# Kernel optimization log

Hardware: AMD Instinct MI355X
Metric: run time of the kernel (lower is better)

## Reference

```python
import jax, jax.numpy as jnp
import numpy as np

KH, KW = 5, 5  # filter_size
PAD_H, PAD_W = KH // 2, KW // 2


def setup_inputs() -> dict:
    key = jax.random.key(0)
    k1, k2 = jax.random.split(key)
    n, c, h, w = 4, 3, 180, 320
    filter_prod = KH * KW          # 25
    upsampling_square = 16
    x = jax.random.normal(k1, (n, c, h, w), dtype=jnp.float32)
    filters = jax.random.uniform(k2, (n, filter_prod, upsampling_square, h, w), dtype=jnp.float32)
    return {"x": x, "filters": filters}


def _unfold(x):
    # Equivalent of conv2d with a grouped identity (eye) expansion filter:
    # extracts kh*kw patches per channel in row-major (i, j) kernel order.
    n, c, h, w = x.shape
    xp = jnp.pad(x, ((0, 0), (0, 0), (PAD_H, PAD_H), (PAD_W, PAD_W)))
    # (n, c, kh*kw, h, w); fixed 25-iteration loop over kernel taps.
    patches = jnp.stack(
        [xp[:, :, i:i + h, j:j + w] for i in range(KH) for j in range(KW)],
        axis=2,
    )
    return patches


def reference(x, filters):
    n, filter_prod, upsampling_square, h, w = filters.shape
    patches = _unfold(x)  # (n, 3, filter_prod, h, w)
    out = jnp.einsum('ncphw,npuhw->ncuhw', patches, filters)
    return out.reshape(n, 3 * upsampling_square, h, w)
```

## Files before the change

kernel.cpp:

```cpp
#include <hip/hip_runtime.h>


#define HH 180
#define WW 320
#define CC 3
#define UU 16
#define NN 4

__global__ __launch_bounds__(256) void duf_kernel(
    const float* __restrict__ x,
    const float* __restrict__ filters,
    float* __restrict__ out)
{
    const int HW = HH * WW;
    int idx = blockIdx.x * 256 + threadIdx.x;
    const int total = NN * UU * HW;
    if (idx >= total) return;

    int w = idx % WW;
    int t = idx / WW;
    int h = t % HH;
    t /= HH;
    int u = t % UU;
    int n = t / UU;

    const float* fptr = filters + ((size_t)((n * 25) * UU + u) * HH + h) * WW + w;
    const float* xbase = x + (size_t)(n * CC) * HW;

    float acc0 = 0.f, acc1 = 0.f, acc2 = 0.f;

    #pragma unroll
    for (int i = 0; i < 5; ++i) {
        int hi = h + i - 2;
        bool rowv = (hi >= 0) & (hi < HH);
        int hic = min(max(hi, 0), HH - 1);
        #pragma unroll
        for (int j = 0; j < 5; ++j) {
            int wj = w + j - 2;
            bool v = rowv & (wj >= 0) & (wj < WW);
            int wjc = min(max(wj, 0), WW - 1);
            int p = i * 5 + j;

            float f = fptr[(size_t)p * UU * HW];
            int xo = hic * WW + wjc;
            float v0 = xbase[xo];
            float v1 = xbase[HW + xo];
            float v2 = xbase[2 * HW + xo];
            if (!v) { v0 = 0.f; v1 = 0.f; v2 = 0.f; }
            acc0 += v0 * f;
            acc1 += v1 * f;
            acc2 += v2 * f;
        }
    }

    float* optr = out + ((size_t)(n * CC * UU + u) * HH + h) * WW + w;
    optr[0]                  = acc0;
    optr[(size_t)UU * HW]     = acc1;
    optr[(size_t)2 * UU * HW] = acc2;
}

extern "C" void kernel_launch(void* const* d_in, const int* in_sizes, int n_in,
                              void* d_out, int out_size, void* d_ws, size_t ws_size,
                              hipStream_t stream) {
    const float* x       = (const float*)d_in[0];
    const float* filters = (const float*)d_in[1];
    float* out           = (float*)d_out;

    const int total = NN * UU * HH * WW;
    const int block = 256;
    const int grid = (total + block - 1) / block;
    duf_kernel<<<grid, block, 0, stream>>>(x, filters, out);
}
```

Baseline: 501.9 us.

## Pre-pad input and compute four pixels per thread with float4 loads

Adds a kernel that writes a zero-padded copy of x into workspace, so the main kernel needs no bounds checks. Each thread now computes four adjacent output pixels. It loads filters and x rows as float4 and reuses one 8-wide x row across the five horizontal taps. This targets the per-element scalar loads and branching on the filter stream, which dominates traffic. In exchange it adds an extra launch and a small pad pass, and it relies on the workspace being large enough and on aligned float4 addresses.

```diff
diff --git a/kernel.cpp b/kernel.cpp
--- a/kernel.cpp
+++ b/kernel.cpp
@@ -6,57 +6,77 @@
 #define CC 3
 #define UU 16
 #define NN 4
+#define HP (HH + 4)
+#define WP 328
+#define HW (HH * WW)
+#define PHW (HP * WP)
+
+__global__ __launch_bounds__(256) void pad_x_kernel(
+    const float* __restrict__ x, float* __restrict__ xpad)
+{
+    int idx = blockIdx.x * 256 + threadIdx.x;
+    int wp = idx % WP;
+    int t  = idx / WP;
+    int hp = t % HP;
+    int nc = t / HP;
+    int h = hp - 2, w = wp - 2;
+    float v = 0.f;
+    if (h >= 0 && h < HH && w >= 0 && w < WW)
+        v = x[(size_t)nc * HW + h * WW + w];
+    xpad[idx] = v;
+}
 
 __global__ __launch_bounds__(256) void duf_kernel(
-    const float* __restrict__ x,
+    const float* __restrict__ xpad,
     const float* __restrict__ filters,
     float* __restrict__ out)
 {
-    const int HW = HH * WW;
     int idx = blockIdx.x * 256 + threadIdx.x;
-    const int total = NN * UU * HW;
-    if (idx >= total) return;
-
-    int w = idx % WW;
-    int t = idx / WW;
-    int h = t % HH;
+    int w4 = idx % (WW / 4);
+    int t  = idx / (WW / 4);
+    int h  = t % HH;
     t /= HH;
     int u = t % UU;
     int n = t / UU;
 
-    const float* fptr = filters + ((size_t)((n * 25) * UU + u) * HH + h) * WW + w;
-    const float* xbase = x + (size_t)(n * CC) * HW;
+    const int wbase = w4 * 4;
+    const float* fptr = filters + (((size_t)n * 25 * UU + u) * HW + (size_t)h * WW + wbase);
 
-    float acc0 = 0.f, acc1 = 0.f, acc2 = 0.f;
+    float acc[CC][4];
+    #pragma unroll
+    for (int c = 0; c < CC; ++c)
+        #pragma unroll
+        for (int q = 0; q < 4; ++q) acc[c][q] = 0.f;
 
     #pragma unroll
     for (int i = 0; i < 5; ++i) {
-        int hi = h + i - 2;
-        bool rowv = (hi >= 0) & (hi < HH);
-        int hic = min(max(hi, 0), HH - 1);
+        float xv[CC][8];
+        #pragma unroll
+        for (int c = 0; c < CC; ++c) {
+            const float* xr = xpad + ((size_t)(n * CC + c) * HP + (h + i)) * WP + wbase;
+            float4 a = *(const float4*)xr;
+            float4 b = *(const float4*)(xr + 4);
+            xv[c][0] = a.x; xv[c][1] = a.y; xv[c][2] = a.z; xv[c][3] = a.w;
+            xv[c][4] = b.x; xv[c][5] = b.y; xv[c][6] = b.z; xv[c][7] = b.w;
+        }
         #pragma unroll
         for (int j = 0; j < 5; ++j) {
-            int wj = w + j - 2;
-            bool v = rowv & (wj >= 0) & (wj < WW);
-            int wjc = min(max(wj, 0), WW - 1);
-            int p = i * 5 + j;
-
-            float f = fptr[(size_t)p * UU * HW];
-            int xo = hic * WW + wjc;
-            float v0 = xbase[xo];
-            float v1 = xbase[HW + xo];
-            float v2 = xbase[2 * HW + xo];
-            if (!v) { v0 = 0.f; v1 = 0.f; v2 = 0.f; }
-            acc0 += v0 * f;
-            acc1 += v1 * f;
-            acc2 += v2 * f;
+            float4 f = *(const float4*)(fptr + (size_t)(i * 5 + j) * UU * HW);
+            #pragma unroll
+            for (int c = 0; c < CC; ++c) {
+                acc[c][0] += xv[c][j + 0] * f.x;
+                acc[c][1] += xv[c][j + 1] * f.y;
+                acc[c][2] += xv[c][j + 2] * f.z;
+                acc[c][3] += xv[c][j + 3] * f.w;
+            }
         }
     }
 
-    float* optr = out + ((size_t)(n * CC * UU + u) * HH + h) * WW + w;
-    optr[0]                  = acc0;
-    optr[(size_t)UU * HW]     = acc1;
-    optr[(size_t)2 * UU * HW] = acc2;
+    #pragma unroll
+    for (int c = 0; c < CC; ++c) {
+        float* op = out + (((size_t)n * CC * UU + c * UU + u) * HW + (size_t)h * WW + wbase);
+        *(float4*)op = make_float4(acc[c][0], acc[c][1], acc[c][2], acc[c][3]);
+    }
 }
 
 extern "C" void kernel_launch(void* const* d_in, const int* in_sizes, int n_in,
@@ -65,9 +85,11 @@
     const float* x       = (const float*)d_in[0];
     const float* filters = (const float*)d_in[1];
     float* out           = (float*)d_out;
+    float* xpad          = (float*)d_ws;
 
-    const int total = NN * UU * HH * WW;
-    const int block = 256;
-    const int grid = (total + block - 1) / block;
-    duf_kernel<<<grid, block, 0, stream>>>(x, filters, out);
+    const int pad_total = NN * CC * PHW;
+    pad_x_kernel<<<pad_total / 256, 256, 0, stream>>>(x, xpad);
+
+    const int total = NN * UU * HH * (WW / 4);
+    duf_kernel<<<total / 256, 256, 0, stream>>>(xpad, filters, out);
 }
```

Result: no change. 496.6 us (-1.1%).
